# Kernel tuning notes

Hardware: AMD Instinct MI355X
Metric: run time of the kernel (lower is better)

Reference implementation:

```python
import jax, jax.numpy as jnp
import numpy as np
import math

B, S, D, H, TOPK = 2, 2048, 1024, 16, 8
DK = D // H

def setup_inputs() -> dict:
    key = jax.random.key(0)
    ks = jax.random.split(key, 12)
    s = 1.0 / math.sqrt(D)
    inp = {
        'x':  jax.random.normal(ks[0], (B, S, D), jnp.float32),
        'Wq': jax.random.normal(ks[1], (D, D), jnp.float32) * s,
        'bq': jnp.zeros((D,), jnp.float32),
        'Wk': jax.random.normal(ks[2], (D, D), jnp.float32) * s,
        'bk': jnp.zeros((D,), jnp.float32),
        'Wv': jax.random.normal(ks[3], (D, D), jnp.float32) * s,
        'bv': jnp.zeros((D,), jnp.float32),
        'Wo': jax.random.normal(ks[4], (D, D), jnp.float32) * s,
        'bo': jnp.zeros((D,), jnp.float32),
        'g1': jnp.asarray(0.1, jnp.float32),  # ReZero gate (init 0 in torch; nonzero for a useful baseline)
        'W1': jax.random.normal(ks[5], (4 * D, D), jnp.float32) * s,
        'b1': jnp.zeros((4 * D,), jnp.float32),
        'W2': jax.random.normal(ks[6], (D, 4 * D), jnp.float32) * (1.0 / math.sqrt(4 * D)),
        'b2': jnp.zeros((D,), jnp.float32),
        'g2': jnp.asarray(0.1, jnp.float32),
    }
    return inp

def reference(x, Wq, bq, Wk, bk, Wv, bv, Wo, bo, g1, W1, b1, W2, b2, g2):
    NEG = jnp.asarray(-10000.0, x.dtype)
    # projections (torch Linear: y = x @ W.T + b), split heads -> [B,H,S,DK]
    def heads(y):
        return y.reshape(B, S, H, DK).transpose(0, 2, 1, 3)
    q = heads(x @ Wq.T + bq)
    k = heads(x @ Wk.T + bk)
    v = heads(x @ Wv.T + bv)
    scores = jnp.einsum('bhqd,bhkd->bhqk', q, k) / math.sqrt(DK)  # [B,H,S,S]
    causal = jnp.triu(jnp.ones((S, S), bool), 1)
    scores = jnp.where(causal, NEG, scores)
    # explicit top-k sparsification: keep only top-8 scores per query row
    top, _ = jax.lax.top_k(scores, TOPK)
    vk = top[..., -1:]                      # k-th largest as threshold
    scores = jnp.where(scores < vk, NEG, scores)
    attn = jax.nn.softmax(scores, axis=-1)
    ctx = jnp.einsum('bhqk,bhkd->bhqd', attn, v)
    ctx = ctx.transpose(0, 2, 1, 3).reshape(B, S, D)
    a = ctx @ Wo.T + bo
    # ReZero (eval mode: dropout = identity): y = a*g; y + y
    h = a * g1
    h = h + h
    # FeedForward: gelu (exact erf, torch default)
    f = jax.nn.gelu(h @ W1.T + b1, approximate=False) @ W2.T + b2
    y2 = f * g2
    return y2 + y2
```

## Files before the change

### kernel.cpp

```cpp
#include <hip/hip_runtime.h>
#include <hip/hip_bf16.h>
#include <cstdint>

#define B_ 2
#define S_ 2048
#define D_ 1024
#define H_ 16
#define DK_ 64
#define QK_ELEMS ((size_t)4194304)
#define NROWS 65536
#define TAU 8e-5f

typedef __attribute__((ext_vector_type(8))) short bf16x8;
typedef __attribute__((ext_vector_type(4))) float f32x4;
typedef __attribute__((ext_vector_type(16))) float f32x16;
typedef __attribute__((ext_vector_type(4))) unsigned short us4;

__device__ __forceinline__ unsigned short f2bf(float f){
  unsigned int u = __float_as_uint(f);
  unsigned int r = u + 0x7fffu + ((u >> 16) & 1u);
  return (unsigned short)(r >> 16);
}
__device__ __forceinline__ float bf2f(unsigned short h){
  return __uint_as_float(((unsigned int)h) << 16);
}

__device__ __forceinline__ void gload16(const void* g, void* l){
  __builtin_amdgcn_global_load_lds(
    (__attribute__((address_space(1))) void*)(void*)(g),
    (__attribute__((address_space(3))) void*)(l), 16, 0, 0);
}

__device__ __forceinline__ f32x4 mfma16(bf16x8 a, bf16x8 b, f32x4 c){
  return __builtin_amdgcn_mfma_f32_16x16x32_bf16(a, b, c, 0, 0, 0);
}
__device__ __forceinline__ f32x16 mfma32(bf16x8 a, bf16x8 b, f32x16 c){
  return __builtin_amdgcn_mfma_f32_32x32x16_bf16(a, b, c, 0, 0, 0);
}

__global__ __launch_bounds__(256) void convert_all(
  const float* __restrict__ x,  const float* __restrict__ Wq, const float* __restrict__ Wk,
  const float* __restrict__ Wv, const float* __restrict__ Wo, const float* __restrict__ W1,
  const float* __restrict__ W2,
  unsigned short* __restrict__ xh, unsigned short* __restrict__ xl,
  unsigned short* __restrict__ Wqkh, unsigned short* __restrict__ Wqkl,
  unsigned short* __restrict__ Wvb, unsigned short* __restrict__ Wob,
  unsigned short* __restrict__ W1b, unsigned short* __restrict__ W2b)
{
  const long total = 16777216 / 4;
  for (long i = (long)blockIdx.x * blockDim.x + threadIdx.x; i < total;
       i += (long)gridDim.x * blockDim.x) {
    long e = i * 4;
    const float* src; unsigned short* dh; unsigned short* dl = nullptr; long o;
    if      (e < 4194304)  { src = x;  dh = xh;            dl = xl;            o = e; }
    else if (e < 5242880)  { src = Wq; dh = Wqkh;          dl = Wqkl;          o = e - 4194304; }
    else if (e < 6291456)  { src = Wk; dh = Wqkh + 1048576; dl = Wqkl + 1048576; o = e - 5242880; }
    else if (e < 7340032)  { src = Wv; dh = Wvb;           o = e - 6291456; }
    else if (e < 8388608)  { src = Wo; dh = Wob;           o = e - 7340032; }
    else if (e < 12582912) { src = W1; dh = W1b;           o = e - 8388608; }
    else                   { src = W2; dh = W2b;           o = e - 12582912; }
    float4 v = *(const float4*)(src + o);
    us4 h;
    h.x = f2bf(v.x); h.y = f2bf(v.y); h.z = f2bf(v.z); h.w = f2bf(v.w);
    *(us4*)(dh + o) = h;
    if (dl) {
      us4 L;
      L.x = f2bf(v.x - bf2f(h.x));
      L.y = f2bf(v.y - bf2f(h.y));
      L.z = f2bf(v.z - bf2f(h.z));
      L.w = f2bf(v.w - bf2f(h.w));
      *(us4*)(dl + o) = L;
    }
  }
}

#define EPI_QK   0
#define EPI_V    1
#define EPI_WO   2
#define EPI_GELU 3
#define EPI_OUT  4

template<int NT, int EPI>
__global__ __launch_bounds__(256) void gemm_bt(
  const unsigned short* __restrict__ A,  const unsigned short* __restrict__ Alo,
  const unsigned short* __restrict__ Bm, const unsigned short* __restrict__ Blo,
  int M, int N, int K,
  const float* __restrict__ bias0, const float* __restrict__ bias1,
  const float* __restrict__ gsc,
  void* __restrict__ out0, void* __restrict__ out1)
{
  constexpr int NTILES = (NT > 1) ? 4 : 2;
  __shared__ char lds[NTILES * 8192];
  char* Ahl = lds;
  char* Bhl = lds + 8192;
  char* All = lds + 16384;
  char* Bll = lds + 24576;
  const int tid = threadIdx.x;
  const int wid = tid >> 6, lane = tid & 63;
  const int mtile = blockIdx.y, ntile = blockIdx.x;
  const int wm = wid >> 1, wn = wid & 1;

  f32x4 acc[4][4];
  #pragma unroll
  for (int i = 0; i < 4; i++)
    #pragma unroll
    for (int j = 0; j < 4; j++)
      #pragma unroll
      for (int r = 0; r < 4; r++) acc[i][j][r] = 0.f;

  const unsigned short* Abase  = A  + (size_t)(mtile * 128) * K;
  const unsigned short* Bbase  = Bm + (size_t)(ntile * 128) * K;
  const unsigned short* Albase = (NT > 1) ? Alo + (size_t)(mtile * 128) * K : nullptr;
  const unsigned short* Blbase = (NT > 1) ? Blo + (size_t)(ntile * 128) * K : nullptr;

  auto stage = [&](char* ldst, const unsigned short* gsrc, int kb){
    #pragma unroll
    for (int j = 0; j < 2; j++){
      int seg = wid + 4 * j;
      int row = seg * 16 + (lane >> 2);
      int c   = (lane & 3) ^ ((row >> 1) & 3);
      gload16(gsrc + (size_t)row * K + kb + c * 8, ldst + seg * 1024);
    }
  };

  for (int kb = 0; kb < K; kb += 32){
    stage(Ahl, Abase, kb);
    stage(Bhl, Bbase, kb);
    if (NT > 1){ stage(All, Albase, kb); stage(Bll, Blbase, kb); }
    __syncthreads();

    bf16x8 af[4], bfr[4], afl[4], bfl[4];
    #pragma unroll
    for (int i = 0; i < 4; i++){
      int ra = wm * 64 + i * 16 + (lane & 15);
      int oa = ra * 64 + (((lane >> 4) ^ ((ra >> 1) & 3)) * 16);
      af[i] = *(const bf16x8*)(Ahl + oa);
      if (NT > 1) afl[i] = *(const bf16x8*)(All + oa);
      int rb = wn * 64 + i * 16 + (lane & 15);
      int ob = rb * 64 + (((lane >> 4) ^ ((rb >> 1) & 3)) * 16);
      bfr[i] = *(const bf16x8*)(Bhl + ob);
      if (NT > 1) bfl[i] = *(const bf16x8*)(Bll + ob);
    }
    #pragma unroll
    for (int i = 0; i < 4; i++)
      #pragma unroll
      for (int j = 0; j < 4; j++){
        if (NT > 1){
          acc[i][j] = mfma16(afl[i], bfl[j], acc[i][j]);
          acc[i][j] = mfma16(afl[i], bfr[j], acc[i][j]);
          acc[i][j] = mfma16(af[i],  bfl[j], acc[i][j]);
        }
        acc[i][j] = mfma16(af[i], bfr[j], acc[i][j]);
      }
    __syncthreads();
  }

  float g2x = 1.0f;
  if (EPI == EPI_WO || EPI == EPI_OUT) g2x = 2.0f * gsc[0];

  #pragma unroll
  for (int j = 0; j < 4; j++){
    int n = ntile * 128 + wn * 64 + j * 16 + (lane & 15);
    float bn;
    if (EPI == EPI_QK) bn = (n < 1024) ? bias0[n] : bias1[n - 1024];
    else               bn = bias0[n];
    #pragma unroll
    for (int i = 0; i < 4; i++){
      int mb = mtile * 128 + wm * 64 + i * 16 + ((lane >> 4) << 2);
      #pragma unroll
      for (int r = 0; r < 4; r++){
        int m = mb + r;
        float val = acc[i][j][r] + bn;
        if (EPI == EPI_QK){
          if (n < 1024) val *= 0.125f;
          int dd = n & 63, hh = (n >> 6) & 15, isK = n >> 10;
          size_t off = ((size_t)((m >> 11) * H_ + hh) * S_ + (m & 2047)) * DK_ + dd
                       + (size_t)isK * QK_ELEMS;
          unsigned short hi = f2bf(val);
          ((unsigned short*)out0)[off] = hi;
          ((unsigned short*)out1)[off] = f2bf(val - bf2f(hi));
        } else if (EPI == EPI_V){
          int dd = n & 63, hh = n >> 6;
          size_t off = ((size_t)((m >> 11) * H_ + hh) * S_ + (m & 2047)) * DK_ + dd;
          ((float*)out0)[off] = val;
        } else if (EPI == EPI_WO){
          ((unsigned short*)out0)[(size_t)m * 1024 + n] = f2bf(val * g2x);
        } else if (EPI == EPI_GELU){
          float t = 0.5f * val * (1.0f + erff(val * 0.70710678118654752f));
          ((unsigned short*)out0)[(size_t)m * 4096 + n] = f2bf(t);
        } else {
          ((float*)out0)[(size_t)m * 1024 + n] = val * g2x;
        }
      }
    }
  }
}

template<int NK>
__device__ __forceinline__ void topk_insert(float (&tv)[NK], int (&ti)[NK],
                                            float& minv, int& minslot, float s, int kidx){
  #pragma unroll
  for (int j = 0; j < NK; j++){
    bool sel = (j == minslot);
    tv[j] = sel ? s    : tv[j];
    ti[j] = sel ? kidx : ti[j];
  }
  minv = tv[0]; minslot = 0;
  #pragma unroll
  for (int j = 1; j < NK; j++){
    bool lt = tv[j] < minv;
    minv    = lt ? tv[j] : minv;
    minslot = lt ? j     : minslot;
  }
}

__global__ __launch_bounds__(256) void attn_topk(
  const unsigned short* __restrict__ QKh, const unsigned short* __restrict__ QKl,
  const float* __restrict__ Vf, unsigned short* __restrict__ ctxb,
  int* __restrict__ cand, unsigned int* __restrict__ flags)
{
  __shared__ char lds[16384];
  const int tid = threadIdx.x, wid = tid >> 6, lane = tid & 63;
  const int b = blockIdx.z, h = blockIdx.y, qt = blockIdx.x;
  const int bh = b * H_ + h;
  const size_t base = (size_t)bh * S_ * DK_;
  const unsigned short* qh = QKh + base;
  const unsigned short* ql = QKl + base;
  const unsigned short* kh = QKh + QK_ELEMS + base;
  const unsigned short* kl = QKl + QK_ELEMS + base;
  const int Q0  = qt * 128;
  const int q0w = Q0 + wid * 32;
  const int qg  = q0w + (lane & 31);

  bf16x8 qfh[4], qfl[4];
  #pragma unroll
  for (int kk = 0; kk < 4; kk++){
    size_t o = (size_t)(q0w + (lane & 31)) * DK_ + kk * 16 + (lane >> 5) * 8;
    qfh[kk] = *(const bf16x8*)(qh + o);
    qfl[kk] = *(const bf16x8*)(ql + o);
  }

  float tv[12]; int ti[12];
  #pragma unroll
  for (int j = 0; j < 12; j++){ tv[j] = -1e30f; ti[j] = -1; }
  float minv = -1e30f; int minslot = 0;

  const int nblocks = (Q0 + 128) >> 6;
  for (int blk = 0; blk < nblocks; ++blk){
    const int kb = blk * 64;
    #pragma unroll
    for (int j = 0; j < 4; j++){
      int segall = wid * 4 + j;
      int tI  = segall >> 3;
      int seg = segall & 7;
      int row = seg * 8 + (lane >> 3);
      int c   = (lane & 7) ^ (row & 7);
      const unsigned short* src = (tI ? kl : kh) + (size_t)(kb + row) * DK_ + c * 8;
      gload16(src, lds + tI * 8192 + seg * 1024);
    }
    __syncthreads();

    if (kb <= q0w + 31){
      #pragma unroll
      for (int sub = 0; sub < 2; ++sub){
        f32x16 acc;
        #pragma unroll
        for (int r = 0; r < 16; r++) acc[r] = 0.f;
        const int key_l = sub * 32 + (lane & 31);
        #pragma unroll
        for (int kk = 0; kk < 4; kk++){
          int cl  = kk * 2 + (lane >> 5);
          int off = key_l * 128 + ((cl ^ (key_l & 7)) * 16);
          bf16x8 ah = *(const bf16x8*)(lds + off);
          bf16x8 al = *(const bf16x8*)(lds + 8192 + off);
          acc = mfma32(al, qfl[kk], acc);
          acc = mfma32(al, qfh[kk], acc);
          acc = mfma32(ah, qfl[kk], acc);
          acc = mfma32(ah, qfh[kk], acc);
        }
        const int krow0 = kb + sub * 32 + ((lane >> 5) << 2);
        #pragma unroll
        for (int r = 0; r < 16; r++){
          float s = acc[r];
          int kidx = krow0 + (r & 3) + ((r >> 2) << 3);
          if ((kidx <= qg) && (s > minv))
            topk_insert(tv, ti, minv, minslot, s, kidx);
        }
      }
    }
    __syncthreads();
  }

  {
    float sv[12]; int si[12];
    #pragma unroll
    for (int j = 0; j < 12; j++){ sv[j] = tv[j]; si[j] = ti[j]; }
    #pragma unroll
    for (int j = 0; j < 12; j++){
      float ov = __shfl_xor(sv[j], 32);
      int   oi = __shfl_xor(si[j], 32);
      if (ov > minv) topk_insert(tv, ti, minv, minslot, ov, oi);
    }
  }

  float t8v[9]; int t8i[9];
  {
    float sv[12]; int si[12];
    #pragma unroll
    for (int j = 0; j < 12; j++){ sv[j] = tv[j]; si[j] = ti[j]; }
    #pragma unroll
    for (int r = 0; r < 9; r++){
      float m = sv[0];
      #pragma unroll
      for (int j = 1; j < 12; j++) m = fmaxf(m, sv[j]);
      int jidx = 0x7fffffff;
      #pragma unroll
      for (int j = 0; j < 12; j++) if (sv[j] == m) jidx = min(jidx, si[j]);
      #pragma unroll
      for (int j = 0; j < 12; j++) if (sv[j] == m && si[j] == jidx) sv[j] = -3e30f;
      t8v[r] = m; t8i[r] = jidx;
    }
  }

  if (lane < 32){
    int row = bh * S_ + qg;
    #pragma unroll
    for (int c = 0; c < 12; c++) cand[row * 12 + c] = ti[c];
    flags[row] = (qg >= 8 && (t8v[7] - t8v[8] < TAU)) ? 1u : 0u;
  }

  float m = t8v[0];
  float w[8]; float Z = 0.f;
  #pragma unroll
  for (int j = 0; j < 8; j++){ w[j] = __expf(t8v[j] - m); Z += w[j]; }
  float inv = 1.0f / Z;

  float cacc[32];
  #pragma unroll
  for (int t = 0; t < 32; t++) cacc[t] = 0.f;
  const int half = lane >> 5;
  const float* vb = Vf + base + half * 32;
  #pragma unroll 2
  for (int j = 0; j < 8; j++){
    float p = w[j] * inv;
    int idx = t8i[j] < 0 ? 0 : t8i[j];
    const float4* vp = (const float4*)(vb + (size_t)idx * DK_);
    #pragma unroll
    for (int t = 0; t < 8; t++){
      float4 vv = vp[t];
      cacc[4*t+0] += p * vv.x; cacc[4*t+1] += p * vv.y;
      cacc[4*t+2] += p * vv.z; cacc[4*t+3] += p * vv.w;
    }
  }

  unsigned short* dst = ctxb + ((size_t)b * S_ + qg) * D_ + h * DK_ + half * 32;
  #pragma unroll
  for (int t = 0; t < 4; t++){
    union { unsigned short u[8]; uint4 v; } pk;
    #pragma unroll
    for (int e = 0; e < 8; e++) pk.u[e] = f2bf(cacc[8*t + e]);
    *(uint4*)(dst + 8*t) = pk.v;
  }
}

__global__ __launch_bounds__(256) void rescue(
  const float* __restrict__ x, const float* __restrict__ Wq, const float* __restrict__ bq,
  const float* __restrict__ Wk, const float* __restrict__ bk,
  const float* __restrict__ Vf, const int* __restrict__ cand,
  const unsigned int* __restrict__ flags, unsigned short* __restrict__ ctxb)
{
  const int row = blockIdx.x * 4 + (threadIdx.x >> 6);
  if (!flags[row]) return;
  const int lane = threadIdx.x & 63;
  const int b = row >> 15, h = (row >> 11) & 15, q = row & 2047;

  int ci[12];
  const float* xc[12];
  #pragma unroll
  for (int c = 0; c < 12; c++){
    int k0 = cand[row * 12 + c];
    ci[c] = k0;
    int ki = (k0 < 0 || k0 > q) ? 0 : k0;
    xc[c] = x + ((size_t)b * S_ + ki) * D_;
  }
  const float* xr  = x  + ((size_t)b * S_ + q) * D_;
  const float* wqr = Wq + (size_t)(h * DK_ + lane) * D_;
  const float* wkr = Wk + (size_t)(h * DK_ + lane) * D_;

  double qd = 0.0, sc[12];
  #pragma unroll
  for (int c = 0; c < 12; c++) sc[c] = 0.0;

  for (int e = 0; e < D_; e += 8){
    float4 wq0 = *(const float4*)(wqr + e), wq1 = *(const float4*)(wqr + e + 4);
    float4 wk0 = *(const float4*)(wkr + e), wk1 = *(const float4*)(wkr + e + 4);
    float4 x0  = *(const float4*)(xr  + e), x1  = *(const float4*)(xr  + e + 4);
    qd += ((double)x0.x * wq0.x + (double)x0.y * wq0.y)
        + ((double)x0.z * wq0.z + (double)x0.w * wq0.w)
        + ((double)x1.x * wq1.x + (double)x1.y * wq1.y)
        + ((double)x1.z * wq1.z + (double)x1.w * wq1.w);
    #pragma unroll
    for (int c = 0; c < 12; c++){
      float4 a0 = *(const float4*)(xc[c] + e), a1 = *(const float4*)(xc[c] + e + 4);
      sc[c] += ((double)a0.x * wk0.x + (double)a0.y * wk0.y)
             + ((double)a0.z * wk0.z + (double)a0.w * wk0.w)
             + ((double)a1.x * wk1.x + (double)a1.y * wk1.y)
             + ((double)a1.z * wk1.z + (double)a1.w * wk1.w);
    }
  }

  const double qdt = qd + (double)bq[h * DK_ + lane];
  const double bkd = (double)bk[h * DK_ + lane];
  double scf[12];
  #pragma unroll
  for (int c = 0; c < 12; c++){
    double p = qdt * (sc[c] + bkd);
    p += __shfl_xor(p, 1);  p += __shfl_xor(p, 2);  p += __shfl_xor(p, 4);
    p += __shfl_xor(p, 8);  p += __shfl_xor(p, 16); p += __shfl_xor(p, 32);
    scf[c] = (ci[c] < 0 || ci[c] > q) ? -1e30 : p * 0.125;
  }

  double t8v[8]; int t8i[8];
  #pragma unroll
  for (int r = 0; r < 8; r++){
    double m = scf[0];
    #pragma unroll
    for (int j = 1; j < 12; j++) m = fmax(m, scf[j]);
    int jidx = 0x7fffffff;
    #pragma unroll
    for (int j = 0; j < 12; j++) if (scf[j] == m) jidx = min(jidx, ci[j]);
    #pragma unroll
    for (int j = 0; j < 12; j++) if (scf[j] == m && ci[j] == jidx) scf[j] = -3e30;
    t8v[r] = m; t8i[r] = jidx;
  }

  float w8[8]; float Z = 0.f;
  #pragma unroll
  for (int j = 0; j < 8; j++){
    w8[j] = __expf((float)(t8v[j] - t8v[0]));
    Z += w8[j];
  }
  float inv = 1.0f / Z;

  const float* vb = Vf + (size_t)(b * H_ + h) * S_ * DK_;
  float acc = 0.f;
  #pragma unroll
  for (int j = 0; j < 8; j++){
    int idx = t8i[j] < 0 ? 0 : t8i[j];
    acc += (w8[j] * inv) * vb[(size_t)idx * DK_ + lane];
  }
  ctxb[((size_t)b * S_ + q) * D_ + h * DK_ + lane] = f2bf(acc);
}

extern "C" void kernel_launch(void* const* d_in, const int* in_sizes, int n_in,
                              void* d_out, int out_size, void* d_ws, size_t ws_size,
                              hipStream_t stream)
{
  const float* x  = (const float*)d_in[0];
  const float* Wq = (const float*)d_in[1];
  const float* bq = (const float*)d_in[2];
  const float* Wk = (const float*)d_in[3];
  const float* bk = (const float*)d_in[4];
  const float* Wv = (const float*)d_in[5];
  const float* bv = (const float*)d_in[6];
  const float* Wo = (const float*)d_in[7];
  const float* bo = (const float*)d_in[8];
  const float* g1 = (const float*)d_in[9];
  const float* W1 = (const float*)d_in[10];
  const float* b1 = (const float*)d_in[11];
  const float* W2 = (const float*)d_in[12];
  const float* b2 = (const float*)d_in[13];
  const float* g2 = (const float*)d_in[14];
  float* out = (float*)d_out;
  char* ws = (char*)d_ws;

  size_t o = 0;
  auto take = [&](size_t bytes){ size_t r = o; o += (bytes + 255) & ~(size_t)255; return r; };
  unsigned short* xh   = (unsigned short*)(ws + take(8388608));
  unsigned short* xl   = (unsigned short*)(ws + take(8388608));
  unsigned short* QKh  = (unsigned short*)(ws + take(16777216));
  unsigned short* QKl  = (unsigned short*)(ws + take(16777216));
  unsigned short* Wqkh = (unsigned short*)(ws + take(4194304));
  unsigned short* Wqkl = (unsigned short*)(ws + take(4194304));
  unsigned short* Wvb  = (unsigned short*)(ws + take(2097152));
  unsigned short* Wob  = (unsigned short*)(ws + take(2097152));
  unsigned short* W1b  = (unsigned short*)(ws + take(8388608));
  unsigned short* W2b  = (unsigned short*)(ws + take(8388608));
  float*          Vf   = (float*)(ws + take(16777216));
  unsigned short* ctxb = (unsigned short*)(ws + take(8388608));
  unsigned short* ub   = (unsigned short*)(ws + take(8388608));
  int*            cand = (int*)(ws + take((size_t)NROWS * 12 * 4));
  unsigned int*   flg  = (unsigned int*)(ws + take((size_t)NROWS * 4));
  unsigned short* tb   = (unsigned short*)ws;

  convert_all<<<2048, 256, 0, stream>>>(x, Wq, Wk, Wv, Wo, W1, W2,
                                        xh, xl, Wqkh, Wqkl, Wvb, Wob, W1b, W2b);
  gemm_bt<4, EPI_QK><<<dim3(16, 32), 256, 0, stream>>>(
      xh, xl, Wqkh, Wqkl, 4096, 2048, 1024, bq, bk, nullptr, QKh, QKl);
  gemm_bt<1, EPI_V><<<dim3(8, 32), 256, 0, stream>>>(
      xh, nullptr, Wvb, nullptr, 4096, 1024, 1024, bv, nullptr, nullptr, Vf, nullptr);
  attn_topk<<<dim3(16, 16, 2), 256, 0, stream>>>(QKh, QKl, Vf, ctxb, cand, flg);
  rescue<<<dim3(NROWS / 4), 256, 0, stream>>>(x, Wq, bq, Wk, bk, Vf, cand, flg, ctxb);
  gemm_bt<1, EPI_WO><<<dim3(8, 32), 256, 0, stream>>>(
      ctxb, nullptr, Wob, nullptr, 4096, 1024, 1024, bo, nullptr, g1, ub, nullptr);
  gemm_bt<1, EPI_GELU><<<dim3(32, 32), 256, 0, stream>>>(
      ub, nullptr, W1b, nullptr, 4096, 4096, 1024, b1, nullptr, nullptr, tb, nullptr);
  gemm_bt<1, EPI_OUT><<<dim3(8, 32), 256, 0, stream>>>(
      tb, nullptr, W2b, nullptr, 4096, 1024, 4096, b2, nullptr, g2, out, nullptr);
}
```

Measured before the change: 1.063 ms.

## Split rescue kernel candidate work across four waves per flagged row

The rescue kernel now uses one 256-thread block per attention row instead of one wave per row. Each of the four waves computes the fp64 key dot products for 3 of the 12 candidates, and the scores are gathered through shared memory before wave 0 does top-8 selection and the V gather. This shortens the serial per-row chain and cuts register pressure from 12 fp64 accumulators to 3. The cost is a 4x larger grid whose blocks mostly exit early, the query dot product being computed redundantly by all four waves, and a block-level barrier.

```diff
diff --git a/kernel.cpp b/kernel.cpp
--- a/kernel.cpp
+++ b/kernel.cpp
@@ -363,93 +363,116 @@
   }
 }
 
-__global__ __launch_bounds__(256) void rescue(
+__global__ __launch_bounds__(256, 1) void rescue(
   const float* __restrict__ x, const float* __restrict__ Wq, const float* __restrict__ bq,
   const float* __restrict__ Wk, const float* __restrict__ bk,
   const float* __restrict__ Vf, const int* __restrict__ cand,
   const unsigned int* __restrict__ flags, unsigned short* __restrict__ ctxb)
 {
-  const int row = blockIdx.x * 4 + (threadIdx.x >> 6);
+  const int row = blockIdx.x;
   if (!flags[row]) return;
-  const int lane = threadIdx.x & 63;
+  __shared__ double scL[12];
+  __shared__ int    ciL[12];
+  const int tid = threadIdx.x, wid = tid >> 6, lane = tid & 63;
   const int b = row >> 15, h = (row >> 11) & 15, q = row & 2047;
 
-  int ci[12];
-  const float* xc[12];
-  #pragma unroll
-  for (int c = 0; c < 12; c++){
-    int k0 = cand[row * 12 + c];
-    ci[c] = k0;
-    int ki = (k0 < 0 || k0 > q) ? 0 : k0;
-    xc[c] = x + ((size_t)b * S_ + ki) * D_;
+  int ci0, ci1, ci2;
+  {
+    const int cb = row * 12 + wid * 3;
+    ci0 = cand[cb + 0]; ci1 = cand[cb + 1]; ci2 = cand[cb + 2];
   }
   const float* xr  = x  + ((size_t)b * S_ + q) * D_;
   const float* wqr = Wq + (size_t)(h * DK_ + lane) * D_;
   const float* wkr = Wk + (size_t)(h * DK_ + lane) * D_;
-
-  double qd = 0.0, sc[12];
-  #pragma unroll
-  for (int c = 0; c < 12; c++) sc[c] = 0.0;
-
+  const float* xp0 = x + ((size_t)b * S_ + ((ci0 < 0 || ci0 > q) ? 0 : ci0)) * D_;
+  const float* xp1 = x + ((size_t)b * S_ + ((ci1 < 0 || ci1 > q) ? 0 : ci1)) * D_;
+  const float* xp2 = x + ((size_t)b * S_ + ((ci2 < 0 || ci2 > q) ? 0 : ci2)) * D_;
+
+  double qd = 0.0, s0d = 0.0, s1d = 0.0, s2d = 0.0;
   for (int e = 0; e < D_; e += 8){
     float4 wq0 = *(const float4*)(wqr + e), wq1 = *(const float4*)(wqr + e + 4);
     float4 wk0 = *(const float4*)(wkr + e), wk1 = *(const float4*)(wkr + e + 4);
-    float4 x0  = *(const float4*)(xr  + e), x1  = *(const float4*)(xr  + e + 4);
-    qd += ((double)x0.x * wq0.x + (double)x0.y * wq0.y)
-        + ((double)x0.z * wq0.z + (double)x0.w * wq0.w)
-        + ((double)x1.x * wq1.x + (double)x1.y * wq1.y)
-        + ((double)x1.z * wq1.z + (double)x1.w * wq1.w);
-    #pragma unroll
-    for (int c = 0; c < 12; c++){
-      float4 a0 = *(const float4*)(xc[c] + e), a1 = *(const float4*)(xc[c] + e + 4);
-      sc[c] += ((double)a0.x * wk0.x + (double)a0.y * wk0.y)
-             + ((double)a0.z * wk0.z + (double)a0.w * wk0.w)
-             + ((double)a1.x * wk1.x + (double)a1.y * wk1.y)
-             + ((double)a1.z * wk1.z + (double)a1.w * wk1.w);
-    }
+    float4 xq0 = *(const float4*)(xr  + e), xq1 = *(const float4*)(xr  + e + 4);
+    float4 c0a = *(const float4*)(xp0 + e), c0b = *(const float4*)(xp0 + e + 4);
+    float4 c1a = *(const float4*)(xp1 + e), c1b = *(const float4*)(xp1 + e + 4);
+    float4 c2a = *(const float4*)(xp2 + e), c2b = *(const float4*)(xp2 + e + 4);
+    qd  += ((double)xq0.x * wq0.x + (double)xq0.y * wq0.y)
+         + ((double)xq0.z * wq0.z + (double)xq0.w * wq0.w)
+         + ((double)xq1.x * wq1.x + (double)xq1.y * wq1.y)
+         + ((double)xq1.z * wq1.z + (double)xq1.w * wq1.w);
+    s0d += ((double)c0a.x * wk0.x + (double)c0a.y * wk0.y)
+         + ((double)c0a.z * wk0.z + (double)c0a.w * wk0.w)
+         + ((double)c0b.x * wk1.x + (double)c0b.y * wk1.y)
+         + ((double)c0b.z * wk1.z + (double)c0b.w * wk1.w);
+    s1d += ((double)c1a.x * wk0.x + (double)c1a.y * wk0.y)
+         + ((double)c1a.z * wk0.z + (double)c1a.w * wk0.w)
+         + ((double)c1b.x * wk1.x + (double)c1b.y * wk1.y)
+         + ((double)c1b.z * wk1.z + (double)c1b.w * wk1.w);
+    s2d += ((double)c2a.x * wk0.x + (double)c2a.y * wk0.y)
+         + ((double)c2a.z * wk0.z + (double)c2a.w * wk0.w)
+         + ((double)c2b.x * wk1.x + (double)c2b.y * wk1.y)
+         + ((double)c2b.z * wk1.z + (double)c2b.w * wk1.w);
   }
 
   const double qdt = qd + (double)bq[h * DK_ + lane];
   const double bkd = (double)bk[h * DK_ + lane];
-  double scf[12];
-  #pragma unroll
-  for (int c = 0; c < 12; c++){
-    double p = qdt * (sc[c] + bkd);
-    p += __shfl_xor(p, 1);  p += __shfl_xor(p, 2);  p += __shfl_xor(p, 4);
-    p += __shfl_xor(p, 8);  p += __shfl_xor(p, 16); p += __shfl_xor(p, 32);
-    scf[c] = (ci[c] < 0 || ci[c] > q) ? -1e30 : p * 0.125;
-  }
-
-  double t8v[8]; int t8i[8];
-  #pragma unroll
-  for (int r = 0; r < 8; r++){
-    double m = scf[0];
-    #pragma unroll
-    for (int j = 1; j < 12; j++) m = fmax(m, scf[j]);
-    int jidx = 0x7fffffff;
-    #pragma unroll
-    for (int j = 0; j < 12; j++) if (scf[j] == m) jidx = min(jidx, ci[j]);
-    #pragma unroll
-    for (int j = 0; j < 12; j++) if (scf[j] == m && ci[j] == jidx) scf[j] = -3e30;
-    t8v[r] = m; t8i[r] = jidx;
-  }
-
-  float w8[8]; float Z = 0.f;
-  #pragma unroll
-  for (int j = 0; j < 8; j++){
-    w8[j] = __expf((float)(t8v[j] - t8v[0]));
-    Z += w8[j];
-  }
-  float inv = 1.0f / Z;
-
-  const float* vb = Vf + (size_t)(b * H_ + h) * S_ * DK_;
-  float acc = 0.f;
-  #pragma unroll
-  for (int j = 0; j < 8; j++){
-    int idx = t8i[j] < 0 ? 0 : t8i[j];
-    acc += (w8[j] * inv) * vb[(size_t)idx * DK_ + lane];
-  }
-  ctxb[((size_t)b * S_ + q) * D_ + h * DK_ + lane] = f2bf(acc);
+  {
+    double p0 = qdt * (s0d + bkd);
+    double p1 = qdt * (s1d + bkd);
+    double p2 = qdt * (s2d + bkd);
+    #pragma unroll
+    for (int d = 1; d < 64; d <<= 1){
+      p0 += __shfl_xor(p0, d);
+      p1 += __shfl_xor(p1, d);
+      p2 += __shfl_xor(p2, d);
+    }
+    if (lane == 0){
+      scL[wid * 3 + 0] = (ci0 < 0 || ci0 > q) ? -1e30 : p0 * 0.125;
+      scL[wid * 3 + 1] = (ci1 < 0 || ci1 > q) ? -1e30 : p1 * 0.125;
+      scL[wid * 3 + 2] = (ci2 < 0 || ci2 > q) ? -1e30 : p2 * 0.125;
+      ciL[wid * 3 + 0] = ci0;
+      ciL[wid * 3 + 1] = ci1;
+      ciL[wid * 3 + 2] = ci2;
+    }
+  }
+  __syncthreads();
+
+  if (wid == 0){
+    double scf[12]; int cif[12];
+    #pragma unroll
+    for (int j = 0; j < 12; j++){ scf[j] = scL[j]; cif[j] = ciL[j]; }
+
+    double t8v[8]; int t8i[8];
+    #pragma unroll
+    for (int r = 0; r < 8; r++){
+      double m = scf[0];
+      #pragma unroll
+      for (int j = 1; j < 12; j++) m = fmax(m, scf[j]);
+      int jidx = 0x7fffffff;
+      #pragma unroll
+      for (int j = 0; j < 12; j++) if (scf[j] == m) jidx = min(jidx, cif[j]);
+      #pragma unroll
+      for (int j = 0; j < 12; j++) if (scf[j] == m && cif[j] == jidx) scf[j] = -3e30;
+      t8v[r] = m; t8i[r] = jidx;
+    }
+
+    float w8[8]; float Z = 0.f;
+    #pragma unroll
+    for (int j = 0; j < 8; j++){
+      w8[j] = __expf((float)(t8v[j] - t8v[0]));
+      Z += w8[j];
+    }
+    float inv = 1.0f / Z;
+
+    const float* vb = Vf + (size_t)(b * H_ + h) * S_ * DK_;
+    float acc = 0.f;
+    #pragma unroll
+    for (int j = 0; j < 8; j++){
+      int idx = t8i[j] < 0 ? 0 : t8i[j];
+      acc += (w8[j] * inv) * vb[(size_t)idx * DK_ + lane];
+    }
+    ctxb[((size_t)b * S_ + q) * D_ + h * DK_ + lane] = f2bf(acc);
+  }
 }
 
 extern "C" void kernel_launch(void* const* d_in, const int* in_sizes, int n_in,
@@ -500,7 +523,7 @@
   gemm_bt<1, EPI_V><<<dim3(8, 32), 256, 0, stream>>>(
       xh, nullptr, Wvb, nullptr, 4096, 1024, 1024, bv, nullptr, nullptr, Vf, nullptr);
   attn_topk<<<dim3(16, 16, 2), 256, 0, stream>>>(QKh, QKl, Vf, ctxb, cand, flg);
-  rescue<<<dim3(NROWS / 4), 256, 0, stream>>>(x, Wq, bq, Wk, bk, Vf, cand, flg, ctxb);
+  rescue<<<dim3(NROWS), 256, 0, stream>>>(x, Wq, bq, Wk, bk, Vf, cand, flg, ctxb);
   gemm_bt<1, EPI_WO><<<dim3(8, 32), 256, 0, stream>>>(
       ctxb, nullptr, Wob, nullptr, 4096, 1024, 1024, bo, nullptr, g1, ub, nullptr);
   gemm_bt<1, EPI_GELU><<<dim3(32, 32), 256, 0, stream>>>(
```

Result: faster. 908.1 us (-14.6%).
